# Kernel tuning notes

Measured on AMD Instinct MI355X. Metric: run time of the kernel, lower is better.

The kernel has to match this reference:

```python
import jax, jax.numpy as jnp
import numpy as np

N_NODES = 50000
N_EDGES = 800000
NFEAT, NHID, NCLASS = 512, 128, 16


def _with_self_loops(edge_idx, n):
    loop = jnp.arange(n, dtype=edge_idx.dtype)
    src = jnp.concatenate([edge_idx[0], loop])  # [E+N]
    dst = jnp.concatenate([edge_idx[1], loop])
    return src, dst


def gcn_conv(x, src, dst, W, b, n):
    # GCNConv with add aggregation, self-loops, symmetric normalization.
    h = x @ W  # [N, out]
    ones = jnp.ones(src.shape[0], dtype=h.dtype)
    deg = jax.ops.segment_sum(ones, dst, num_segments=n)  # in-degree incl. self-loops
    dinv = jnp.where(deg > 0, jax.lax.rsqrt(deg), 0.0)
    norm = dinv[src] * dinv[dst]  # [E+N]
    msg = h[src] * norm[:, None]  # gather + scale
    out = jax.ops.segment_sum(msg, dst, num_segments=n)  # scatter-add
    return out + b


def setup_inputs() -> dict:
    key = jax.random.key(0)
    ks = jax.random.split(key, 8)
    x = jax.random.normal(ks[0], (N_NODES, NFEAT), dtype=jnp.float32)
    edge_idx = jax.random.randint(ks[1], (2, N_EDGES), 0, N_NODES, dtype=jnp.int64)
    s1 = 1.0 / np.sqrt(NFEAT)
    s2 = 1.0 / np.sqrt(NHID)
    W1 = jax.random.uniform(ks[2], (NFEAT, NHID), jnp.float32, -s1, s1)
    b1 = jnp.zeros((NHID,), jnp.float32)
    W2 = jax.random.uniform(ks[3], (NHID, NHID), jnp.float32, -s2, s2)
    b2 = jnp.zeros((NHID,), jnp.float32)
    Wc = jax.random.uniform(ks[4], (NHID, NCLASS), jnp.float32, -s2, s2)
    bc = jax.random.uniform(ks[5], (NCLASS,), jnp.float32, -s2, s2)
    return {"x": x, "edge_idx": edge_idx, "W1": W1, "b1": b1, "W2": W2, "b2": b2, "Wc": Wc, "bc": bc}


def reference(x, edge_idx, W1, b1, W2, b2, Wc, bc):
    n = x.shape[0]
    src, dst = _with_self_loops(edge_idx, n)
    h = gcn_conv(x, src, dst, W1, b1, n)
    h = jax.nn.relu(h)  # dropout is identity in eval mode
    h = gcn_conv(h, src, dst, W2, b2, n)
    h = jax.nn.relu(h)
    logits = h @ Wc + bc
    return jax.nn.log_softmax(logits, axis=1)
```

## Files before the change

kernel.cpp:

```cpp
#include <hip/hip_runtime.h>
#include <math.h>

#define NFEAT 512
#define NHID  128
#define NCLASS 16
#define SCAN_BS 512
#define AGG_BLOCKS 2048

typedef __attribute__((ext_vector_type(8))) short short8;
typedef __attribute__((ext_vector_type(4))) float f32x4;

static __device__ __forceinline__ ushort f2b(float f) {
    union { float f; uint u; } v; v.f = f;
    uint r = v.u + 0x7FFFu + ((v.u >> 16) & 1u);
    return (ushort)(r >> 16);
}
static __device__ __forceinline__ float b2f_lo(uint bits) {
    union { uint u; float f; } v; v.u = bits << 16; return v.f;
}
static __device__ __forceinline__ float b2f_hi(uint bits) {
    union { uint u; float f; } v; v.u = bits & 0xffff0000u; return v.f;
}


__global__ void k_init_tcast(const float* __restrict__ W1, const float* __restrict__ W2,
                             ushort* __restrict__ W1T, ushort* __restrict__ W2T,
                             int* __restrict__ deg, int n) {
    int idx = blockIdx.x * 256 + threadIdx.x;
    if (idx < n) deg[idx] = 1;
    if (idx < NFEAT * 128) {
        int k = idx >> 7, c = idx & 127;
        W1T[(size_t)c * NFEAT + k] = f2b(W1[idx]);
    } else {
        int j = idx - NFEAT * 128;
        if (j < NHID * 128) {
            int k = j >> 7, c = j & 127;
            W2T[(size_t)c * NHID + k] = f2b(W2[j]);
        }
    }
}

__global__ void k_count(const int* __restrict__ dst, int e, int* __restrict__ deg) {
    int i = blockIdx.x * blockDim.x + threadIdx.x;
    if (i < e) atomicAdd(&deg[dst[i]], 1);
}

__global__ void k_scan1(const int* __restrict__ deg, float* __restrict__ dinv,
                        int* __restrict__ cursor, int* __restrict__ offs,
                        int* __restrict__ bsum, int n) {
    __shared__ int s[SCAN_BS];
    int t = threadIdx.x;
    int i = blockIdx.x * SCAN_BS + t;
    int d = (i < n) ? deg[i] : 0;
    if (i < n) { dinv[i] = rsqrtf((float)d); cursor[i] = 0; }
    int v = (i < n) ? ((d + 7) >> 3) : 0;
    s[t] = v;
    for (int off = 1; off < SCAN_BS; off <<= 1) {
        __syncthreads();
        int x = (t >= off) ? s[t - off] : 0;
        __syncthreads();
        s[t] += x;
    }
    __syncthreads();
    if (i < n) offs[i] = s[t] - v;
    if (t == SCAN_BS - 1) bsum[blockIdx.x] = s[t];
}

__global__ void k_scan2(int* __restrict__ bsum, int* __restrict__ offs, int nb, int n) {
    int lane = threadIdx.x;
    int carry = 0;
    for (int base = 0; base < nb; base += 64) {
        int i = base + lane;
        int v = (i < nb) ? bsum[i] : 0;
        int orig = v;
        for (int off = 1; off < 64; off <<= 1) {
            int t = __shfl_up(v, off);
            if (lane >= off) v += t;
        }
        if (i < nb) bsum[i] = carry + v - orig;
        carry += __shfl(v, 63);
    }
    if (lane == 0) offs[n] = carry;
}

__global__ void k_scan3(int* __restrict__ offs, const int* __restrict__ bsum, int n) {
    int i = blockIdx.x * SCAN_BS + threadIdx.x;
    if (i < n) offs[i] += bsum[blockIdx.x];
}

__global__ void k_fill_edges(const int* __restrict__ src, const int* __restrict__ dst, int e,
                             const int* __restrict__ goffs, int* __restrict__ cursor,
                             uint* __restrict__ colp32) {
    int i = blockIdx.x * blockDim.x + threadIdx.x;
    if (i < e) {
        int d = dst[i];
        int p = atomicAdd(&cursor[d], 1);
        colp32[(size_t)goffs[d] * 8 + p] = (uint)src[i];
    }
}

__global__ void k_fill_tail(const int* __restrict__ goffs, const int* __restrict__ deg,
                            uint* __restrict__ colp32, ushort* __restrict__ hs, int n) {
    int i = blockIdx.x * blockDim.x + threadIdx.x;
    if (i < 128) {
        int s = i >> 5, f = i & 31;
        hs[((size_t)s * (n + 1) + n) * 32 + f] = 0;
    }
    if (i < n) {
        int g0 = goffs[i], g1 = goffs[i + 1];
        size_t base = (size_t)g0 * 8;
        int d = deg[i];
        int slots = (g1 - g0) * 8;
        colp32[base + d - 1] = (uint)i;
        for (int p = d; p < slots; p++) colp32[base + p] = (uint)n;
        uint meta = (uint)(i + 1) << 16;
        for (int k = slots - 8; k < slots; k++) colp32[base + k] |= meta;
        if (i == 0) {
            int G = goffs[n];
            for (int k = 0; k < 48; k++) colp32[(size_t)G * 8 + k] = (uint)n;
        }
    }
}

__global__ void k_rankstart(const uint* __restrict__ colp32, const int* __restrict__ goffs,
                            int* __restrict__ rankgs, int n) {
    int r = blockIdx.x * blockDim.x + threadIdx.x;
    if (r >= AGG_BLOCKS) return;
    int G = goffs[n];
    int run = (G + AGG_BLOCKS - 1) / AGG_BLOCKS;
    int g = r * run;
    int ge = g + run; if (ge > G) ge = G;
    if (g >= G) { rankgs[r] = -1; return; }
    if (g > 0) {
        while (g < ge && !(colp32[(size_t)(g - 1) * 8] >> 16)) g++;
        if (g >= ge) { rankgs[r] = -1; return; }
    }
    rankgs[r] = g;
}


template<int A_F32>
__global__ __launch_bounds__(256) void k_gemm(const void* __restrict__ Aptr,
                                              const ushort* __restrict__ WT,
                                              const float* __restrict__ rowscale,
                                              ushort* __restrict__ Hs, int M, int K) {
    __shared__ ushort As[64][40];
    __shared__ ushort Bs[128][40];

    const int tid = threadIdx.x;
    const int wc = tid >> 6, lane = tid & 63;
    const int lr = lane & 15, lk = (lane >> 4) * 8;
    const int rowbase = blockIdx.x * 64;

    f32x4 acc[4][2];
#pragma unroll
    for (int i = 0; i < 4; i++)
#pragma unroll
        for (int j = 0; j < 2; j++) acc[i][j] = (f32x4)0.f;

    const int sr = tid >> 2;
    const int sh = (tid & 3) * 8;

    for (int k0 = 0; k0 < K; k0 += 32) {
        {
            int gr = rowbase + sr;
            ushort tmp[8];
            if (A_F32) {
                const float* A = (const float*)Aptr;
                if (gr < M) {
                    const float* p = A + (size_t)gr * K + k0 + sh;
#pragma unroll
                    for (int q = 0; q < 2; q++) {
                        float4 v = *(const float4*)(p + q * 4);
                        tmp[q * 4 + 0] = f2b(v.x); tmp[q * 4 + 1] = f2b(v.y);
                        tmp[q * 4 + 2] = f2b(v.z); tmp[q * 4 + 3] = f2b(v.w);
                    }
                } else {
#pragma unroll
                    for (int q = 0; q < 8; q++) tmp[q] = 0;
                }
            } else {
                const ushort* A = (const ushort*)Aptr;
                if (gr < M) {
                    *(short8*)&tmp[0] = *(const short8*)(A + (size_t)gr * K + k0 + sh);
                } else {
#pragma unroll
                    for (int q = 0; q < 8; q++) tmp[q] = 0;
                }
            }
            *(short8*)&As[sr][sh] = *(short8*)&tmp[0];
        }
        {
#pragma unroll
            for (int t = 0; t < 2; t++) {
                int c = tid + t * 256;
                int row = c >> 2, q = c & 3;
                short8 v = *(const short8*)(WT + (size_t)row * K + k0 + q * 8);
                *(short8*)&Bs[row][q * 8] = v;
            }
        }
        __syncthreads();

        short8 af[4], bfv[2];
#pragma unroll
        for (int i = 0; i < 4; i++) af[i] = *(const short8*)&As[i * 16 + lr][lk];
#pragma unroll
        for (int j = 0; j < 2; j++) bfv[j] = *(const short8*)&Bs[wc * 32 + j * 16 + lr][lk];
#pragma unroll
        for (int i = 0; i < 4; i++)
#pragma unroll
            for (int j = 0; j < 2; j++)
                acc[i][j] = __builtin_amdgcn_mfma_f32_16x16x32_bf16(af[i], bfv[j], acc[i][j], 0, 0, 0);
        __syncthreads();
    }

#pragma unroll
    for (int i = 0; i < 4; i++) {
#pragma unroll
        for (int r = 0; r < 4; r++) {
            int row = rowbase + i * 16 + (lane >> 4) * 4 + r;
            if (row < M) {
                float sc = rowscale[row];
#pragma unroll
                for (int j = 0; j < 2; j++) {
                    int f = j * 16 + lr;
                    Hs[((size_t)wc * (M + 1) + row) * 32 + f] = f2b(acc[i][j][r] * sc);
                }
            }
        }
    }
}


__global__ __launch_bounds__(256) void k_aggs(const ushort* __restrict__ hs,
                                              const uint* __restrict__ colp32,
                                              const int* __restrict__ rankgs,
                                              const int* __restrict__ goffs,
                                              const float* __restrict__ dinv,
                                              const float* __restrict__ bias,
                                              ushort* __restrict__ outp, int n) {
    const int b = blockIdx.x;
    const int s = (b & 7) >> 1;
    const int wid = threadIdx.x >> 6, lane = threadIdx.x & 63;
    const int e8 = lane >> 3, q = lane & 7;

    const int G = goffs[n];
    const int rank = ((b >> 3) * 2 + (b & 1)) * 4 + wid;
    const int run = (G + AGG_BLOCKS - 1) / AGG_BLOCKS;
    int gs = rankgs[rank];
    int ge = (rank + 1) * run; if (ge > G) ge = G;
    if (gs < 0 || gs >= ge) return;

    const ushort* hsl = hs + (size_t)s * (n + 1) * 32;
    const float4 bv = *(const float4*)(bias + s * 32 + q * 4);

    int g = gs;
    const uint* cp = colp32 + (size_t)g * 8 + e8;
    uint cw0 = cp[0], cw1 = cp[8], cw2 = cp[16], cw3 = cp[24];
    uint2 pk0 = *(const uint2*)(hsl + (size_t)(cw0 & 0xffffu) * 32 + q * 4);
    uint2 pk1 = *(const uint2*)(hsl + (size_t)(cw1 & 0xffffu) * 32 + q * 4);
    uint2 pk2 = *(const uint2*)(hsl + (size_t)(cw2 & 0xffffu) * 32 + q * 4);
    float fdv0 = (cw0 >> 16) ? dinv[(cw0 >> 16) - 1] : 0.f;
    float fdv1 = (cw1 >> 16) ? dinv[(cw1 >> 16) - 1] : 0.f;
    float fdv2 = (cw2 >> 16) ? dinv[(cw2 >> 16) - 1] : 0.f;
    float a0 = 0.f, a1 = 0.f, a2 = 0.f, a3 = 0.f;

    while (true) {
        uint cw4 = cp[32];
        uint2 pk3 = *(const uint2*)(hsl + (size_t)(cw3 & 0xffffu) * 32 + q * 4);
        float fdv3 = (cw3 >> 16) ? dinv[(cw3 >> 16) - 1] : 0.f;

        a0 += b2f_lo(pk0.x); a1 += b2f_hi(pk0.x);
        a2 += b2f_lo(pk0.y); a3 += b2f_hi(pk0.y);

        if (cw0 >> 16) {
            int v = (int)(cw0 >> 16) - 1;
            float r0 = a0, r1 = a1, r2 = a2, r3 = a3;
#pragma unroll
            for (int off = 8; off <= 32; off <<= 1) {
                r0 += __shfl_xor(r0, off); r1 += __shfl_xor(r1, off);
                r2 += __shfl_xor(r2, off); r3 += __shfl_xor(r3, off);
            }
            r0 = fmaxf(fmaf(r0, fdv0, bv.x), 0.f);
            r1 = fmaxf(fmaf(r1, fdv0, bv.y), 0.f);
            r2 = fmaxf(fmaf(r2, fdv0, bv.z), 0.f);
            r3 = fmaxf(fmaf(r3, fdv0, bv.w), 0.f);
            if (lane < 8) {
                uint2 u;
                u.x = (uint)f2b(r0) | ((uint)f2b(r1) << 16);
                u.y = (uint)f2b(r2) | ((uint)f2b(r3) << 16);
                *(uint2*)(outp + (size_t)v * 128 + s * 32 + q * 4) = u;
            }
            if (g + 1 >= ge) break;
            a0 = a1 = a2 = a3 = 0.f;
        }
        g++; cp += 8;
        cw0 = cw1; cw1 = cw2; cw2 = cw3; cw3 = cw4;
        pk0 = pk1; pk1 = pk2; pk2 = pk3;
        fdv0 = fdv1; fdv1 = fdv2; fdv2 = fdv3;
    }
}


__global__ __launch_bounds__(256) void k_classify(const ushort* __restrict__ h,
                                                  const float* __restrict__ Wc,
                                                  const float* __restrict__ bc,
                                                  float* __restrict__ out, int n) {
    __shared__ float Ws[128 * 16];
    int tid = threadIdx.x;
#pragma unroll
    for (int t = 0; t < 8; t++) Ws[tid + 256 * t] = Wc[tid + 256 * t];
    __syncthreads();

    int wid = tid >> 6, lane = tid & 63;
    int v = blockIdx.x * 4 + wid;
    if (v >= n) return;

    int j = lane & 15, c = lane >> 4;
    const ushort* hv = h + (size_t)v * 128 + c * 32;
    float acc = 0.f;
#pragma unroll
    for (int t = 0; t < 16; t++) {
        uint pk = *(const uint*)(hv + t * 2);
        acc = fmaf(b2f_lo(pk), Ws[(c * 32 + t * 2 + 0) * 16 + j], acc);
        acc = fmaf(b2f_hi(pk), Ws[(c * 32 + t * 2 + 1) * 16 + j], acc);
    }
    acc += __shfl_xor(acc, 16);
    acc += __shfl_xor(acc, 32);
    acc += bc[j];

    float m = acc;
#pragma unroll
    for (int o = 8; o >= 1; o >>= 1) m = fmaxf(m, __shfl_xor(m, o));
    float sum = expf(acc - m);
#pragma unroll
    for (int o = 8; o >= 1; o >>= 1) sum += __shfl_xor(sum, o);
    if (lane < 16) out[(size_t)v * 16 + j] = acc - m - logf(sum);
}


extern "C" void kernel_launch(void* const* d_in, const int* in_sizes, int n_in,
                              void* d_out, int out_size, void* d_ws, size_t ws_size,
                              hipStream_t stream) {
    const float* x  = (const float*)d_in[0];
    const int* eidx = (const int*)d_in[1];
    const float* W1 = (const float*)d_in[2];
    const float* b1 = (const float*)d_in[3];
    const float* W2 = (const float*)d_in[4];
    const float* b2 = (const float*)d_in[5];
    const float* Wc = (const float*)d_in[6];
    const float* bc = (const float*)d_in[7];
    float* out = (float*)d_out;

    const int N = in_sizes[0] / NFEAT;
    const int E = in_sizes[1] / 2;
    const int* src = eidx;
    const int* dst = eidx + E;

    char* p = (char*)d_ws;
    auto alloc = [&](size_t bytes) { char* r = p; p += (bytes + 255) & ~(size_t)255; return r; };
    int*    deg    = (int*)   alloc((size_t)N * 4);
    float*  dinv   = (float*) alloc((size_t)N * 4);
    int*    goffs  = (int*)   alloc((size_t)(N + 1) * 4);
    int*    cursor = (int*)   alloc((size_t)N * 4);
    uint*   colp32 = (uint*)  alloc(((size_t)E + 8ull * N + 64) * 4);
    int*    rankgs = (int*)   alloc((size_t)AGG_BLOCKS * 4);
    int*    bsum   = (int*)   alloc((size_t)256 * 4);
    ushort* W1T    = (ushort*)alloc((size_t)128 * NFEAT * 2);
    ushort* W2T    = (ushort*)alloc((size_t)128 * NHID * 2);
    ushort* hs     = (ushort*)alloc((size_t)(N + 1) * NHID * 2);
    ushort* g1     = (ushort*)alloc((size_t)N * NHID * 2);
    ushort* g2     = (ushort*)alloc((size_t)N * NHID * 2);

    const int nb = (N + SCAN_BS - 1) / SCAN_BS;

    k_init_tcast<<<((NFEAT + NHID) * 128 + 255) / 256, 256, 0, stream>>>(W1, W2, W1T, W2T, deg, N);
    k_count<<<(E + 255) / 256, 256, 0, stream>>>(dst, E, deg);
    k_scan1<<<nb, SCAN_BS, 0, stream>>>(deg, dinv, cursor, goffs, bsum, N);
    k_scan2<<<1, 64, 0, stream>>>(bsum, goffs, nb, N);
    k_scan3<<<nb, SCAN_BS, 0, stream>>>(goffs, bsum, N);
    k_fill_edges<<<(E + 255) / 256, 256, 0, stream>>>(src, dst, E, goffs, cursor, colp32);
    k_fill_tail<<<(N + 255) / 256, 256, 0, stream>>>(goffs, deg, colp32, hs, N);
    k_rankstart<<<(AGG_BLOCKS + 255) / 256, 256, 0, stream>>>(colp32, goffs, rankgs, N);

    const int gblocks = (N + 63) / 64;
    k_gemm<1><<<gblocks, 256, 0, stream>>>(x, W1T, dinv, hs, N, NFEAT);
    k_aggs<<<AGG_BLOCKS, 256, 0, stream>>>(hs, colp32, rankgs, goffs, dinv, b1, g1, N);
    k_gemm<0><<<gblocks, 256, 0, stream>>>(g1, W2T, dinv, hs, N, NHID);
    k_aggs<<<AGG_BLOCKS, 256, 0, stream>>>(hs, colp32, rankgs, goffs, dinv, b2, g2, N);
    k_classify<<<(N + 3) / 4, 256, 0, stream>>>(g2, Wc, bc, out, N);
}
```

Before: 261.6 us.

## Replace padded 8-slot CSR groups with compact edge streams per 4-lane group

Drops the padding of each node's neighbour list to multiples of 8 and stores a compact CSR of E+N entries, with the end-of-node marker packed into the last entry. The aggregation kernel now gives each 4-lane group its own independent edge stream (16384 streams) that loads 16 bytes per lane, instead of a wavefront walking 8 edges at a time and reducing across lanes with shuffles. This removes the padding traffic, the dummy zero row, the fill_tail kernel and the cross-lane reductions. In exchange, lanes within a wavefront diverge and hit imbalance at node boundaries, and gathers from different streams are less coalesced.

```diff
diff --git a/kernel.cpp b/kernel.cpp
--- a/kernel.cpp
+++ b/kernel.cpp
@@ -5,7 +5,8 @@
 #define NHID  128
 #define NCLASS 16
 #define SCAN_BS 512
-#define AGG_BLOCKS 2048
+#define AGG_BLOCKS 1024
+#define NSTREAMS 16384
 
 typedef __attribute__((ext_vector_type(8))) short short8;
 typedef __attribute__((ext_vector_type(4))) float f32x4;
@@ -53,8 +54,7 @@
     int i = blockIdx.x * SCAN_BS + t;
     int d = (i < n) ? deg[i] : 0;
     if (i < n) { dinv[i] = rsqrtf((float)d); cursor[i] = 0; }
-    int v = (i < n) ? ((d + 7) >> 3) : 0;
-    s[t] = v;
+    s[t] = d;
     for (int off = 1; off < SCAN_BS; off <<= 1) {
         __syncthreads();
         int x = (t >= off) ? s[t - off] : 0;
@@ -62,7 +62,7 @@
         s[t] += x;
     }
     __syncthreads();
-    if (i < n) offs[i] = s[t] - v;
+    if (i < n) offs[i] = s[t] - d;
     if (t == SCAN_BS - 1) bsum[blockIdx.x] = s[t];
 }
 
@@ -89,50 +89,32 @@
 }
 
 __global__ void k_fill_edges(const int* __restrict__ src, const int* __restrict__ dst, int e,
-                             const int* __restrict__ goffs, int* __restrict__ cursor,
-                             uint* __restrict__ colp32) {
+                             const int* __restrict__ eoffs, int* __restrict__ cursor,
+                             uint* __restrict__ colp32, int n, int S) {
     int i = blockIdx.x * blockDim.x + threadIdx.x;
     if (i < e) {
         int d = dst[i];
         int p = atomicAdd(&cursor[d], 1);
-        colp32[(size_t)goffs[d] * 8 + p] = (uint)src[i];
-    }
-}
-
-__global__ void k_fill_tail(const int* __restrict__ goffs, const int* __restrict__ deg,
-                            uint* __restrict__ colp32, ushort* __restrict__ hs, int n) {
-    int i = blockIdx.x * blockDim.x + threadIdx.x;
-    if (i < 128) {
-        int s = i >> 5, f = i & 31;
-        hs[((size_t)s * (n + 1) + n) * 32 + f] = 0;
+        colp32[eoffs[d] + p] = (uint)src[i];
     }
     if (i < n) {
-        int g0 = goffs[i], g1 = goffs[i + 1];
-        size_t base = (size_t)g0 * 8;
-        int d = deg[i];
-        int slots = (g1 - g0) * 8;
-        colp32[base + d - 1] = (uint)i;
-        for (int p = d; p < slots; p++) colp32[base + p] = (uint)n;
-        uint meta = (uint)(i + 1) << 16;
-        for (int k = slots - 8; k < slots; k++) colp32[base + k] |= meta;
-        if (i == 0) {
-            int G = goffs[n];
-            for (int k = 0; k < 48; k++) colp32[(size_t)G * 8 + k] = (uint)n;
-        }
-    }
-}
-
-__global__ void k_rankstart(const uint* __restrict__ colp32, const int* __restrict__ goffs,
-                            int* __restrict__ rankgs, int n) {
+        colp32[eoffs[i + 1] - 1] = (uint)i | ((uint)(i + 1) << 16);
+    }
+    if (i == 0) {
+#pragma unroll
+        for (int k = 0; k < 8; k++) colp32[S + k] = 0;
+    }
+}
+
+__global__ void k_rankstart(const uint* __restrict__ colp32, int* __restrict__ rankgs, int S) {
     int r = blockIdx.x * blockDim.x + threadIdx.x;
-    if (r >= AGG_BLOCKS) return;
-    int G = goffs[n];
-    int run = (G + AGG_BLOCKS - 1) / AGG_BLOCKS;
-    int g = r * run;
-    int ge = g + run; if (ge > G) ge = G;
-    if (g >= G) { rankgs[r] = -1; return; }
+    if (r >= NSTREAMS) return;
+    int len = (S + NSTREAMS - 1) / NSTREAMS;
+    int g = r * len;
+    int ge = g + len; if (ge > S) ge = S;
+    if (g >= S) { rankgs[r] = -1; return; }
     if (g > 0) {
-        while (g < ge && !(colp32[(size_t)(g - 1) * 8] >> 16)) g++;
+        while (g < ge && !(colp32[g - 1] >> 16)) g++;
         if (g >= ge) { rankgs[r] = -1; return; }
     }
     rankgs[r] = g;
@@ -224,7 +206,7 @@
 #pragma unroll
                 for (int j = 0; j < 2; j++) {
                     int f = j * 16 + lr;
-                    Hs[((size_t)wc * (M + 1) + row) * 32 + f] = f2b(acc[i][j][r] * sc);
+                    Hs[((size_t)wc * M + row) * 32 + f] = f2b(acc[i][j][r] * sc);
                 }
             }
         }
@@ -235,69 +217,68 @@
 __global__ __launch_bounds__(256) void k_aggs(const ushort* __restrict__ hs,
                                               const uint* __restrict__ colp32,
                                               const int* __restrict__ rankgs,
-                                              const int* __restrict__ goffs,
                                               const float* __restrict__ dinv,
                                               const float* __restrict__ bias,
-                                              ushort* __restrict__ outp, int n) {
+                                              ushort* __restrict__ outp, int n, int S) {
     const int b = blockIdx.x;
-    const int s = (b & 7) >> 1;
+    const int s = b & 3;
     const int wid = threadIdx.x >> 6, lane = threadIdx.x & 63;
-    const int e8 = lane >> 3, q = lane & 7;
-
-    const int G = goffs[n];
-    const int rank = ((b >> 3) * 2 + (b & 1)) * 4 + wid;
-    const int run = (G + AGG_BLOCKS - 1) / AGG_BLOCKS;
-    int gs = rankgs[rank];
-    int ge = (rank + 1) * run; if (ge > G) ge = G;
-    if (gs < 0 || gs >= ge) return;
-
-    const ushort* hsl = hs + (size_t)s * (n + 1) * 32;
-    const float4 bv = *(const float4*)(bias + s * 32 + q * 4);
-
-    int g = gs;
-    const uint* cp = colp32 + (size_t)g * 8 + e8;
-    uint cw0 = cp[0], cw1 = cp[8], cw2 = cp[16], cw3 = cp[24];
-    uint2 pk0 = *(const uint2*)(hsl + (size_t)(cw0 & 0xffffu) * 32 + q * 4);
-    uint2 pk1 = *(const uint2*)(hsl + (size_t)(cw1 & 0xffffu) * 32 + q * 4);
-    uint2 pk2 = *(const uint2*)(hsl + (size_t)(cw2 & 0xffffu) * 32 + q * 4);
+    const int st16 = lane >> 2, q = lane & 3;
+    const int stream = (((b >> 2) << 2) + wid) * 16 + st16;
+    const int len = (S + NSTREAMS - 1) / NSTREAMS;
+    int gs = rankgs[stream];
+    int ge = (stream + 1) * len; if (ge > S) ge = S;
+    bool alive = (gs >= 0);
+    int g = alive ? gs : 0;
+
+    const ushort* hsl = hs + (size_t)s * n * 32;
+    const float4 bv0 = *(const float4*)(bias + s * 32 + q * 8);
+    const float4 bv1 = *(const float4*)(bias + s * 32 + q * 8 + 4);
+
+    const uint* cp = colp32 + g;
+    uint cw0 = cp[0], cw1 = cp[1], cw2 = cp[2];
+    uint4 pk0 = *(const uint4*)(hsl + (size_t)(cw0 & 0xffffu) * 32 + q * 8);
+    uint4 pk1 = *(const uint4*)(hsl + (size_t)(cw1 & 0xffffu) * 32 + q * 8);
     float fdv0 = (cw0 >> 16) ? dinv[(cw0 >> 16) - 1] : 0.f;
     float fdv1 = (cw1 >> 16) ? dinv[(cw1 >> 16) - 1] : 0.f;
-    float fdv2 = (cw2 >> 16) ? dinv[(cw2 >> 16) - 1] : 0.f;
     float a0 = 0.f, a1 = 0.f, a2 = 0.f, a3 = 0.f;
-
-    while (true) {
-        uint cw4 = cp[32];
-        uint2 pk3 = *(const uint2*)(hsl + (size_t)(cw3 & 0xffffu) * 32 + q * 4);
-        float fdv3 = (cw3 >> 16) ? dinv[(cw3 >> 16) - 1] : 0.f;
-
-        a0 += b2f_lo(pk0.x); a1 += b2f_hi(pk0.x);
-        a2 += b2f_lo(pk0.y); a3 += b2f_hi(pk0.y);
-
-        if (cw0 >> 16) {
-            int v = (int)(cw0 >> 16) - 1;
-            float r0 = a0, r1 = a1, r2 = a2, r3 = a3;
-#pragma unroll
-            for (int off = 8; off <= 32; off <<= 1) {
-                r0 += __shfl_xor(r0, off); r1 += __shfl_xor(r1, off);
-                r2 += __shfl_xor(r2, off); r3 += __shfl_xor(r3, off);
-            }
-            r0 = fmaxf(fmaf(r0, fdv0, bv.x), 0.f);
-            r1 = fmaxf(fmaf(r1, fdv0, bv.y), 0.f);
-            r2 = fmaxf(fmaf(r2, fdv0, bv.z), 0.f);
-            r3 = fmaxf(fmaf(r3, fdv0, bv.w), 0.f);
-            if (lane < 8) {
-                uint2 u;
+    float a4 = 0.f, a5 = 0.f, a6 = 0.f, a7 = 0.f;
+
+    while (__any(alive)) {
+        if (alive) {
+            uint cw3 = cp[3];
+            uint4 pk2 = *(const uint4*)(hsl + (size_t)(cw2 & 0xffffu) * 32 + q * 8);
+            float fdv2 = (cw2 >> 16) ? dinv[(cw2 >> 16) - 1] : 0.f;
+
+            a0 += b2f_lo(pk0.x); a1 += b2f_hi(pk0.x);
+            a2 += b2f_lo(pk0.y); a3 += b2f_hi(pk0.y);
+            a4 += b2f_lo(pk0.z); a5 += b2f_hi(pk0.z);
+            a6 += b2f_lo(pk0.w); a7 += b2f_hi(pk0.w);
+
+            if (cw0 >> 16) {
+                int v = (int)(cw0 >> 16) - 1;
+                float r0 = fmaxf(fmaf(a0, fdv0, bv0.x), 0.f);
+                float r1 = fmaxf(fmaf(a1, fdv0, bv0.y), 0.f);
+                float r2 = fmaxf(fmaf(a2, fdv0, bv0.z), 0.f);
+                float r3 = fmaxf(fmaf(a3, fdv0, bv0.w), 0.f);
+                float r4 = fmaxf(fmaf(a4, fdv0, bv1.x), 0.f);
+                float r5 = fmaxf(fmaf(a5, fdv0, bv1.y), 0.f);
+                float r6 = fmaxf(fmaf(a6, fdv0, bv1.z), 0.f);
+                float r7 = fmaxf(fmaf(a7, fdv0, bv1.w), 0.f);
+                uint4 u;
                 u.x = (uint)f2b(r0) | ((uint)f2b(r1) << 16);
                 u.y = (uint)f2b(r2) | ((uint)f2b(r3) << 16);
-                *(uint2*)(outp + (size_t)v * 128 + s * 32 + q * 4) = u;
+                u.z = (uint)f2b(r4) | ((uint)f2b(r5) << 16);
+                u.w = (uint)f2b(r6) | ((uint)f2b(r7) << 16);
+                *(uint4*)(outp + (size_t)v * 128 + s * 32 + q * 8) = u;
+                a0 = a1 = a2 = a3 = a4 = a5 = a6 = a7 = 0.f;
+                if (g + 1 >= ge) alive = false;
             }
-            if (g + 1 >= ge) break;
-            a0 = a1 = a2 = a3 = 0.f;
-        }
-        g++; cp += 8;
-        cw0 = cw1; cw1 = cw2; cw2 = cw3; cw3 = cw4;
-        pk0 = pk1; pk1 = pk2; pk2 = pk3;
-        fdv0 = fdv1; fdv1 = fdv2; fdv2 = fdv3;
+            g++; cp++;
+            cw0 = cw1; cw1 = cw2; cw2 = cw3;
+            pk0 = pk1; pk1 = pk2;
+            fdv0 = fdv1; fdv1 = fdv2;
+        }
     }
 }
 
@@ -354,6 +335,7 @@
 
     const int N = in_sizes[0] / NFEAT;
     const int E = in_sizes[1] / 2;
+    const int S = E + N;
     const int* src = eidx;
     const int* dst = eidx + E;
 
@@ -361,14 +343,14 @@
     auto alloc = [&](size_t bytes) { char* r = p; p += (bytes + 255) & ~(size_t)255; return r; };
     int*    deg    = (int*)   alloc((size_t)N * 4);
     float*  dinv   = (float*) alloc((size_t)N * 4);
-    int*    goffs  = (int*)   alloc((size_t)(N + 1) * 4);
+    int*    eoffs  = (int*)   alloc((size_t)(N + 1) * 4);
     int*    cursor = (int*)   alloc((size_t)N * 4);
-    uint*   colp32 = (uint*)  alloc(((size_t)E + 8ull * N + 64) * 4);
-    int*    rankgs = (int*)   alloc((size_t)AGG_BLOCKS * 4);
+    uint*   colp32 = (uint*)  alloc(((size_t)S + 16) * 4);
+    int*    rankgs = (int*)   alloc((size_t)NSTREAMS * 4);
     int*    bsum   = (int*)   alloc((size_t)256 * 4);
     ushort* W1T    = (ushort*)alloc((size_t)128 * NFEAT * 2);
     ushort* W2T    = (ushort*)alloc((size_t)128 * NHID * 2);
-    ushort* hs     = (ushort*)alloc((size_t)(N + 1) * NHID * 2);
+    ushort* hs     = (ushort*)alloc((size_t)N * NHID * 2);
     ushort* g1     = (ushort*)alloc((size_t)N * NHID * 2);
     ushort* g2     = (ushort*)alloc((size_t)N * NHID * 2);
 
@@ -376,17 +358,16 @@
 
     k_init_tcast<<<((NFEAT + NHID) * 128 + 255) / 256, 256, 0, stream>>>(W1, W2, W1T, W2T, deg, N);
     k_count<<<(E + 255) / 256, 256, 0, stream>>>(dst, E, deg);
-    k_scan1<<<nb, SCAN_BS, 0, stream>>>(deg, dinv, cursor, goffs, bsum, N);
-    k_scan2<<<1, 64, 0, stream>>>(bsum, goffs, nb, N);
-    k_scan3<<<nb, SCAN_BS, 0, stream>>>(goffs, bsum, N);
-    k_fill_edges<<<(E + 255) / 256, 256, 0, stream>>>(src, dst, E, goffs, cursor, colp32);
-    k_fill_tail<<<(N + 255) / 256, 256, 0, stream>>>(goffs, deg, colp32, hs, N);
-    k_rankstart<<<(AGG_BLOCKS + 255) / 256, 256, 0, stream>>>(colp32, goffs, rankgs, N);
+    k_scan1<<<nb, SCAN_BS, 0, stream>>>(deg, dinv, cursor, eoffs, bsum, N);
+    k_scan2<<<1, 64, 0, stream>>>(bsum, eoffs, nb, N);
+    k_scan3<<<nb, SCAN_BS, 0, stream>>>(eoffs, bsum, N);
+    k_fill_edges<<<(E + 255) / 256, 256, 0, stream>>>(src, dst, E, eoffs, cursor, colp32, N, S);
+    k_rankstart<<<(NSTREAMS + 255) / 256, 256, 0, stream>>>(colp32, rankgs, S);
 
     const int gblocks = (N + 63) / 64;
     k_gemm<1><<<gblocks, 256, 0, stream>>>(x, W1T, dinv, hs, N, NFEAT);
-    k_aggs<<<AGG_BLOCKS, 256, 0, stream>>>(hs, colp32, rankgs, goffs, dinv, b1, g1, N);
+    k_aggs<<<AGG_BLOCKS, 256, 0, stream>>>(hs, colp32, rankgs, dinv, b1, g1, N, S);
     k_gemm<0><<<gblocks, 256, 0, stream>>>(g1, W2T, dinv, hs, N, NHID);
-    k_aggs<<<AGG_BLOCKS, 256, 0, stream>>>(hs, colp32, rankgs, goffs, dinv, b2, g2, N);
+    k_aggs<<<AGG_BLOCKS, 256, 0, stream>>>(hs, colp32, rankgs, dinv, b2, g2, N, S);
     k_classify<<<(N + 3) / 4, 256, 0, stream>>>(g2, Wc, bc, out, N);
 }
```

After: 260.6 us. About the same (-0.4%).
